# Optimization experiments

Hardware: AMD Instinct MI355X
Metric: run time of the kernel (lower is better)

## Reference

```python
import jax, jax.numpy as jnp
import numpy as np

HEAD_SIZE = 64


def setup_inputs() -> dict:
    key = jax.random.key(0)
    ks = jax.random.split(key, 4)
    B, S, H, D = 8, 4096, 768, HEAD_SIZE
    scale = 1.0 / np.sqrt(H)
    return {
        "x": jax.random.normal(ks[0], (B, S, H), dtype=jnp.float32),
        "Wq": jax.random.normal(ks[1], (H, D), dtype=jnp.float32) * scale,
        "bq": jnp.zeros((D,), dtype=jnp.float32),
        "Wk": jax.random.normal(ks[2], (H, D), dtype=jnp.float32) * scale,
        "bk": jnp.zeros((D,), dtype=jnp.float32),
        "Wv": jax.random.normal(ks[3], (H, D), dtype=jnp.float32) * scale,
        "bv": jnp.zeros((D,), dtype=jnp.float32),
    }


def reference(x, Wq, bq, Wk, bk, Wv, bv):
    # x: [B, S, H]
    B, S, H = x.shape
    D = Wq.shape[1]
    q = x @ Wq + bq  # [B, S, D]
    k = x @ Wk + bk
    v = x @ Wv + bv
    # naive full score matrix [B, S, S]
    scores = jnp.einsum("bsd,btd->bst", q, k)
    causal = jnp.tril(jnp.ones((S, S), dtype=bool))  # lower-triangular mask
    scores = jnp.where(causal[None, :, :], scores, -jnp.inf)
    attn = jax.nn.softmax(scores / jnp.sqrt(jnp.float32(D)), axis=-1)
    # dropout is identity in eval/deterministic reference
    out = jnp.einsum("bst,btd->bsd", attn, v)  # [B, S, D]
    return out
```

## Files before the change

### kernel.cpp

```cpp
#include <hip/hip_runtime.h>

typedef unsigned short u16;
typedef __bf16 bf16_t;
typedef bf16_t bf16x8 __attribute__((ext_vector_type(8)));
typedef float f32x4 __attribute__((ext_vector_type(4)));
typedef u16 u16x8 __attribute__((ext_vector_type(8)));
typedef u16 u16x4 __attribute__((ext_vector_type(4)));

#define B_ 8
#define S_ 4096
#define H_ 768
#define M_ (B_ * S_)

__device__ __forceinline__ u16 f2b(float f) {
  unsigned u = __float_as_uint(f);
  u += 0x7fffu + ((u >> 16) & 1u);
  return (u16)(u >> 16);
}

__device__ __forceinline__ void gl_lds16(const void* g, void* l) {
  __builtin_amdgcn_global_load_lds(
      (const __attribute__((address_space(1))) void*)g,
      (__attribute__((address_space(3))) void*)l, 16, 0, 0);
}

__global__ __launch_bounds__(256) void wconv_k(const float* __restrict__ Wq,
                                               const float* __restrict__ Wk,
                                               const float* __restrict__ Wv,
                                               u16* __restrict__ WbT) {
  __shared__ float wt[64 * 68];
  const int tid = threadIdx.x;
  int mat = blockIdx.x / 12;
  int k0 = (blockIdx.x % 12) * 64;
  const float* W = (mat == 0) ? Wq : ((mat == 1) ? Wk : Wv);
  int r = tid >> 2, c0 = (tid & 3) * 16;
  const float* src = W + (size_t)(k0 + r) * 64 + c0;
#pragma unroll
  for (int j = 0; j < 16; j += 4)
    *(float4*)&wt[r * 68 + c0 + j] = *(const float4*)(src + j);
  __syncthreads();
  int d = tid >> 2;
  u16* dst = WbT + (size_t)(mat * 64 + d) * 768 + k0 + c0;
  u16x8 o0, o1;
#pragma unroll
  for (int j = 0; j < 8; ++j) o0[j] = f2b(wt[(c0 + j) * 68 + d]);
#pragma unroll
  for (int j = 0; j < 8; ++j) o1[j] = f2b(wt[(c0 + 8 + j) * 68 + d]);
  *(u16x8*)dst = o0;
  *(u16x8*)(dst + 8) = o1;
}

__global__ __launch_bounds__(256) void qkv_k(const float* __restrict__ x,
                                             const u16* __restrict__ WbT,
                                             const float* __restrict__ bq,
                                             const float* __restrict__ bk,
                                             const float* __restrict__ bv,
                                             u16* __restrict__ qb,
                                             u16* __restrict__ kb,
                                             u16* __restrict__ vbT) {
  __shared__ __align__(16) u16 smem[2 * 2560 + 2 * 7680];
  const int tid = threadIdx.x;
  const int w = tid >> 6, ln = tid & 15, qd = (tid >> 4) & 3;
  const int row0 = blockIdx.x * 64;

  const f32x4 z4 = {0.f, 0.f, 0.f, 0.f};
  f32x4 acc[4][3];
#pragma unroll
  for (int rt = 0; rt < 4; ++rt)
#pragma unroll
    for (int ct = 0; ct < 3; ++ct) acc[rt][ct] = z4;

  const int xr = tid >> 2, xc = (tid & 3) * 8;
  float4 xf0, xf1;
  u16x8 wf[3];

  auto load_t = [&](int kt) {
    const float* sx = x + (size_t)(row0 + xr) * 768 + kt * 32 + xc;
    xf0 = *(const float4*)sx;
    xf1 = *(const float4*)(sx + 4);
#pragma unroll
    for (int i = 0; i < 3; ++i) {
      int c = i * 256 + tid;
      int r = c >> 2, off = (c & 3) * 8;
      wf[i] = *(const u16x8*)(WbT + (size_t)r * 768 + kt * 32 + off);
    }
  };

  load_t(0);
  for (int kt = 0; kt < 24; ++kt) {
    u16* xs = smem + (kt & 1) * 2560;
    u16* wsb = smem + 5120 + (kt & 1) * 7680;
    {
      u16x8 v;
      v[0] = f2b(xf0.x); v[1] = f2b(xf0.y); v[2] = f2b(xf0.z); v[3] = f2b(xf0.w);
      v[4] = f2b(xf1.x); v[5] = f2b(xf1.y); v[6] = f2b(xf1.z); v[7] = f2b(xf1.w);
      *(u16x8*)&xs[xr * 40 + xc] = v;
#pragma unroll
      for (int i = 0; i < 3; ++i) {
        int c = i * 256 + tid;
        int r = c >> 2, off = (c & 3) * 8;
        *(u16x8*)&wsb[r * 40 + off] = wf[i];
      }
    }
    if (kt < 23) load_t(kt + 1);
    __syncthreads();
    bf16x8 af[4], bfr[3];
#pragma unroll
    for (int rt = 0; rt < 4; ++rt)
      af[rt] = *(const bf16x8*)&xs[(rt * 16 + ln) * 40 + qd * 8];
#pragma unroll
    for (int ct = 0; ct < 3; ++ct)
      bfr[ct] = *(const bf16x8*)&wsb[(w * 48 + ct * 16 + ln) * 40 + qd * 8];
#pragma unroll
    for (int rt = 0; rt < 4; ++rt)
#pragma unroll
      for (int ct = 0; ct < 3; ++ct)
        acc[rt][ct] = __builtin_amdgcn_mfma_f32_16x16x32_bf16(
            af[rt], bfr[ct], acc[rt][ct], 0, 0, 0);
    __syncthreads();
  }

  u16* vt = smem;
#pragma unroll
  for (int ct = 0; ct < 3; ++ct) {
    int col = w * 48 + ct * 16 + ln;
    int mat = col >> 6, d = col & 63;
    if (mat < 2) {
      const float* bp = (mat == 0) ? bq : bk;
      u16* op = (mat == 0) ? qb : kb;
      float bias = bp[d];
      float scale = (mat == 0) ? 0.18033688011112042f : 1.0f;
#pragma unroll
      for (int rt = 0; rt < 4; ++rt)
#pragma unroll
        for (int r = 0; r < 4; ++r)
          op[(size_t)(row0 + rt * 16 + qd * 4 + r) * 64 + d] =
              f2b((acc[rt][ct][r] + bias) * scale);
    } else {
      float bias = bv[d];
#pragma unroll
      for (int rt = 0; rt < 4; ++rt)
#pragma unroll
        for (int r = 0; r < 4; ++r)
          vt[d * 72 + rt * 16 + qd * 4 + r] = f2b(acc[rt][ct][r] + bias);
    }
  }
  __syncthreads();
  {
    int d = tid >> 2, so = (tid & 3) * 16;
    int b = row0 >> 12, s0 = row0 & 4095;
    u16* dst = vbT + ((size_t)b * 64 + d) * 4096 + s0 + so;
    *(u16x8*)dst = *(const u16x8*)&vt[d * 72 + so];
    *(u16x8*)(dst + 8) = *(const u16x8*)&vt[d * 72 + so + 8];
  }
}

__global__ __launch_bounds__(256) void attn_k(const u16* __restrict__ qb,
                                              const u16* __restrict__ kb,
                                              const u16* __restrict__ vbT,
                                              float* __restrict__ po,
                                              float* __restrict__ pl) {
  __shared__ __align__(16) u16 ks[3][4096];
  __shared__ __align__(16) u16 vs[3][4096];
  __shared__ __align__(16) u16 ps[4 * 32 * 64];
  const int tid = threadIdx.x;
  const int wv = tid >> 6, ln = tid & 15, qd = (tid >> 4) & 3;
  const int id = blockIdx.x;
  const int b = id & 7;
  const int j = id >> 3;
  int qi = 31, acc = 0;
  while (acc + ((qi >> 3) + 1) <= j) {
    acc += (qi >> 3) + 1;
    --qi;
  }
  const int c = j - acc;
  const int ntiles = 2 * qi + 2;
  const int nc = (qi >> 3) + 1;
  const int bas = ntiles / nc, rem = ntiles % nc;
  const int tstart = c * bas + (c < rem ? c : rem);
  const int tcount = bas + (c < rem ? 1 : 0);
  const int q0 = qi * 128;
  const int q0w = q0 + wv * 32;
  const int base = b * S_;
  const u16* kg = kb + (size_t)base * 64;
  const u16* vg = vbT + (size_t)b * 64 * 4096;

  bf16x8 qf[2][2];
#pragma unroll
  for (int qt = 0; qt < 2; ++qt) {
    const u16* qrow = qb + (size_t)(base + q0w + qt * 16 + ln) * 64;
    qf[qt][0] = *(const bf16x8*)(qrow + qd * 8);
    qf[qt][1] = *(const bf16x8*)(qrow + 32 + qd * 8);
  }
  const f32x4 z4 = {0.f, 0.f, 0.f, 0.f};
  f32x4 o0[4] = {z4, z4, z4, z4};
  f32x4 o1[4] = {z4, z4, z4, z4};
  float lq0 = 0.f, lq1 = 0.f;
  u16* psw = ps + wv * 2048;
  const int sw = (ln & 7) << 3;
  const int lr = (tid & 63) >> 3, csl = tid & 7;

  auto prefetch = [&](int bufi, int tile) {
    const u16* kt_ = kg + (size_t)tile * 4096;
    const u16* vt_ = vg + tile * 64;
#pragma unroll
    for (int i = 0; i < 2; ++i) {
      int r0 = wv * 16 + i * 8;
      int r = r0 + lr;
      int cc = csl ^ (r & 7);
      gl_lds16(kt_ + r * 64 + cc * 8, &ks[bufi][r0 * 64]);
      gl_lds16(vt_ + (size_t)r * 4096 + cc * 8, &vs[bufi][r0 * 64]);
    }
  };

  prefetch(0, tstart);
  prefetch(1, tstart + (tcount > 1 ? 1 : 0));
  int cur = 0, pfb = 2;
  for (int it = 0; it < tcount; ++it) {
    asm volatile("s_waitcnt vmcnt(4)" ::: "memory");
    __builtin_amdgcn_s_barrier();
    int nx = it + 2;
    nx = nx < tcount ? nx : tcount - 1;
    prefetch(pfb, tstart + nx);
    const int t0a = (tstart + it) * 64;

    if (t0a <= q0w + 31) {
      f32x4 s0[4] = {z4, z4, z4, z4};
      f32x4 s1[4] = {z4, z4, z4, z4};
#pragma unroll
      for (int kc = 0; kc < 2; ++kc) {
        int cs = (kc * 4 + qd) ^ (ln & 7);
#pragma unroll
        for (int nt = 0; nt < 4; ++nt) {
          bf16x8 kf = *(const bf16x8*)&ks[cur][(nt * 16 + ln) * 64 + cs * 8];
          s0[nt] = __builtin_amdgcn_mfma_f32_16x16x32_bf16(kf, qf[0][kc], s0[nt], 0, 0, 0);
          s1[nt] = __builtin_amdgcn_mfma_f32_16x16x32_bf16(kf, qf[1][kc], s1[nt], 0, 0, 0);
        }
      }
      if (t0a + 63 > q0w) {
#pragma unroll
        for (int nt = 0; nt < 4; ++nt) {
          int tg = t0a + nt * 16 + qd * 4;
#pragma unroll
          for (int r = 0; r < 4; ++r) {
            if (tg + r > q0w + ln) s0[nt][r] = -INFINITY;
            if (tg + r > q0w + 16 + ln) s1[nt][r] = -INFINITY;
          }
        }
      }
#pragma unroll
      for (int nt = 0; nt < 4; ++nt) {
        u16x4 w0, w1;
#pragma unroll
        for (int r = 0; r < 4; ++r) {
          float p0 = __builtin_amdgcn_exp2f(s0[nt][r]);
          float p1 = __builtin_amdgcn_exp2f(s1[nt][r]);
          lq0 += p0;
          lq1 += p1;
          w0[r] = f2b(p0);
          w1[r] = f2b(p1);
        }
        int off = (nt * 16 + qd * 4) ^ sw;
        *(u16x4*)&psw[ln * 64 + off] = w0;
        *(u16x4*)&psw[(16 + ln) * 64 + off] = w1;
      }
#pragma unroll
      for (int kc = 0; kc < 2; ++kc) {
        int poff = (kc * 32 + qd * 8) ^ sw;
        bf16x8 a0 = *(const bf16x8*)&psw[ln * 64 + poff];
        bf16x8 a1 = *(const bf16x8*)&psw[(16 + ln) * 64 + poff];
        int cs = (kc * 4 + qd) ^ (ln & 7);
#pragma unroll
        for (int nt = 0; nt < 4; ++nt) {
          bf16x8 vf = *(const bf16x8*)&vs[cur][(nt * 16 + ln) * 64 + cs * 8];
          o0[nt] = __builtin_amdgcn_mfma_f32_16x16x32_bf16(a0, vf, o0[nt], 0, 0, 0);
          o1[nt] = __builtin_amdgcn_mfma_f32_16x16x32_bf16(a1, vf, o1[nt], 0, 0, 0);
        }
      }
    }
    cur = (cur == 2) ? 0 : cur + 1;
    pfb = (pfb == 2) ? 0 : pfb + 1;
  }

  lq0 += __shfl_xor(lq0, 16);
  lq0 += __shfl_xor(lq0, 32);
  lq1 += __shfl_xor(lq1, 16);
  lq1 += __shfl_xor(lq1, 32);

  float* op = po + (size_t)c * 2097152;
  float* lpt = pl + (size_t)c * 32768;
#pragma unroll
  for (int r = 0; r < 4; ++r) {
    int row0 = base + q0w + qd * 4 + r;
    int row1 = row0 + 16;
#pragma unroll
    for (int nt = 0; nt < 4; ++nt) {
      op[(size_t)row0 * 64 + nt * 16 + ln] = o0[nt][r];
      op[(size_t)row1 * 64 + nt * 16 + ln] = o1[nt][r];
    }
  }
  if (qd == 0) {
    lpt[base + q0w + ln] = lq0;
    lpt[base + q0w + 16 + ln] = lq1;
  }
}

__global__ __launch_bounds__(256) void comb_k(const float* __restrict__ po,
                                              const float* __restrict__ pl,
                                              float* __restrict__ out) {
  int idx = blockIdx.x * 256 + threadIdx.x;
  int r = idx >> 4, d0 = (idx & 15) * 4;
  int qi = (r & 4095) >> 7;
  int nc = (qi >> 3) + 1;
  const float* p = po + (size_t)r * 64 + d0;
  float4 a = *(const float4*)p;
  float l = pl[r];
  if (nc > 1) {
    float4 t = *(const float4*)(p + 2097152);
    a.x += t.x; a.y += t.y; a.z += t.z; a.w += t.w;
    l += pl[r + 32768];
  }
  if (nc > 2) {
    float4 t = *(const float4*)(p + 4194304);
    a.x += t.x; a.y += t.y; a.z += t.z; a.w += t.w;
    l += pl[r + 65536];
  }
  if (nc > 3) {
    float4 t = *(const float4*)(p + 6291456);
    a.x += t.x; a.y += t.y; a.z += t.z; a.w += t.w;
    l += pl[r + 98304];
  }
  float inv = 1.0f / l;
  a.x *= inv; a.y *= inv; a.z *= inv; a.w *= inv;
  *(float4*)(out + (size_t)r * 64 + d0) = a;
}

extern "C" void kernel_launch(void* const* d_in, const int* in_sizes, int n_in,
                              void* d_out, int out_size, void* d_ws, size_t ws_size,
                              hipStream_t stream) {
  const float* x  = (const float*)d_in[0];
  const float* Wq = (const float*)d_in[1];
  const float* bq = (const float*)d_in[2];
  const float* Wk = (const float*)d_in[3];
  const float* bk = (const float*)d_in[4];
  const float* Wv = (const float*)d_in[5];
  const float* bv = (const float*)d_in[6];
  float* out = (float*)d_out;

  char* wsp = (char*)d_ws;
  u16* WbT = (u16*)wsp;
  u16* qb  = (u16*)(wsp + 294912);
  u16* kb  = (u16*)(wsp + 4489216);
  u16* vbT = (u16*)(wsp + 8683520);
  float* po = (float*)(wsp + 12877824);
  float* pl = (float*)(wsp + 46432256);

  hipLaunchKernelGGL(wconv_k, dim3(36), dim3(256), 0, stream, Wq, Wk, Wv, WbT);
  hipLaunchKernelGGL(qkv_k, dim3(512), dim3(256), 0, stream,
                     x, WbT, bq, bk, bv, qb, kb, vbT);
  hipLaunchKernelGGL(attn_k, dim3(640), dim3(256), 0, stream,
                     qb, kb, vbT, po, pl);
  hipLaunchKernelGGL(comb_k, dim3(2048), dim3(256), 0, stream,
                     po, pl, out);
}
```

Before: 224.6 us.

## Keep softmax probabilities in registers by permuting V^T layout to match MFMA fragments

Removes the per-wave LDS round trip for the bf16 probability tile. The P values are now packed straight from the score accumulators into MFMA A operands with v_cvt_pk_bf16_f32. To make this valid, the projection kernel writes V^T with a permuted sequence order inside each 32-column group, so the register layout of P matches the K dimension of the PV MFMA. It also raises wave priority around the MFMA blocks with s_setprio. This relies on the column permutation being exactly consistent between the two kernels, and it frees the ps LDS buffer.

```diff
diff --git a/kernel.cpp b/kernel.cpp
--- a/kernel.cpp
+++ b/kernel.cpp
@@ -6,6 +6,7 @@
 typedef float f32x4 __attribute__((ext_vector_type(4)));
 typedef u16 u16x8 __attribute__((ext_vector_type(8)));
 typedef u16 u16x4 __attribute__((ext_vector_type(4)));
+typedef unsigned u32x4 __attribute__((ext_vector_type(4)));
 
 #define B_ 8
 #define S_ 4096
@@ -149,9 +150,13 @@
   {
     int d = tid >> 2, so = (tid & 3) * 16;
     int b = row0 >> 12, s0 = row0 & 4095;
-    u16* dst = vbT + ((size_t)b * 64 + d) * 4096 + s0 + so;
-    *(u16x8*)dst = *(const u16x8*)&vt[d * 72 + so];
-    *(u16x8*)(dst + 8) = *(const u16x8*)&vt[d * 72 + so + 8];
+    u16* dst = vbT + ((size_t)b * 64 + d) * 4096 + s0;
+#pragma unroll
+    for (int g = 0; g < 4; ++g) {
+      int ts = so + g * 4;
+      int tn = (ts & 0x23) | ((ts & 4) << 2) | ((ts & 0x18) >> 1);
+      *(u16x4*)(dst + ts) = *(const u16x4*)&vt[d * 72 + tn];
+    }
   }
 }
 
@@ -162,7 +167,6 @@
                                               float* __restrict__ pl) {
   __shared__ __align__(16) u16 ks[3][4096];
   __shared__ __align__(16) u16 vs[3][4096];
-  __shared__ __align__(16) u16 ps[4 * 32 * 64];
   const int tid = threadIdx.x;
   const int wv = tid >> 6, ln = tid & 15, qd = (tid >> 4) & 3;
   const int id = blockIdx.x;
@@ -196,8 +200,6 @@
   f32x4 o0[4] = {z4, z4, z4, z4};
   f32x4 o1[4] = {z4, z4, z4, z4};
   float lq0 = 0.f, lq1 = 0.f;
-  u16* psw = ps + wv * 2048;
-  const int sw = (ln & 7) << 3;
   const int lr = (tid & 63) >> 3, csl = tid & 7;
 
   auto prefetch = [&](int bufi, int tile) {
@@ -227,6 +229,7 @@
     if (t0a <= q0w + 31) {
       f32x4 s0[4] = {z4, z4, z4, z4};
       f32x4 s1[4] = {z4, z4, z4, z4};
+      __builtin_amdgcn_s_setprio(1);
 #pragma unroll
       for (int kc = 0; kc < 2; ++kc) {
         int cs = (kc * 4 + qd) ^ (ln & 7);
@@ -237,6 +240,7 @@
           s1[nt] = __builtin_amdgcn_mfma_f32_16x16x32_bf16(kf, qf[1][kc], s1[nt], 0, 0, 0);
         }
       }
+      __builtin_amdgcn_s_setprio(0);
       if (t0a + 63 > q0w) {
 #pragma unroll
         for (int nt = 0; nt < 4; ++nt) {
@@ -248,27 +252,32 @@
           }
         }
       }
-#pragma unroll
-      for (int nt = 0; nt < 4; ++nt) {
-        u16x4 w0, w1;
+      float p0[4][4], p1[4][4];
+#pragma unroll
+      for (int nt = 0; nt < 4; ++nt)
 #pragma unroll
         for (int r = 0; r < 4; ++r) {
-          float p0 = __builtin_amdgcn_exp2f(s0[nt][r]);
-          float p1 = __builtin_amdgcn_exp2f(s1[nt][r]);
-          lq0 += p0;
-          lq1 += p1;
-          w0[r] = f2b(p0);
-          w1[r] = f2b(p1);
+          p0[nt][r] = __builtin_amdgcn_exp2f(s0[nt][r]);
+          p1[nt][r] = __builtin_amdgcn_exp2f(s1[nt][r]);
+          lq0 += p0[nt][r];
+          lq1 += p1[nt][r];
         }
-        int off = (nt * 16 + qd * 4) ^ sw;
-        *(u16x4*)&psw[ln * 64 + off] = w0;
-        *(u16x4*)&psw[(16 + ln) * 64 + off] = w1;
-      }
+      unsigned pk0[8], pk1[8];
+#pragma unroll
+      for (int i = 0; i < 8; ++i) {
+        int nt = i >> 1, rb = (i & 1) * 2;
+        asm("v_cvt_pk_bf16_f32 %0, %1, %2"
+            : "=v"(pk0[i]) : "v"(p0[nt][rb]), "v"(p0[nt][rb + 1]));
+        asm("v_cvt_pk_bf16_f32 %0, %1, %2"
+            : "=v"(pk1[i]) : "v"(p1[nt][rb]), "v"(p1[nt][rb + 1]));
+      }
+      __builtin_amdgcn_s_setprio(1);
 #pragma unroll
       for (int kc = 0; kc < 2; ++kc) {
-        int poff = (kc * 32 + qd * 8) ^ sw;
-        bf16x8 a0 = *(const bf16x8*)&psw[ln * 64 + poff];
-        bf16x8 a1 = *(const bf16x8*)&psw[(16 + ln) * 64 + poff];
+        u32x4 w0 = {pk0[4 * kc], pk0[4 * kc + 1], pk0[4 * kc + 2], pk0[4 * kc + 3]};
+        u32x4 w1 = {pk1[4 * kc], pk1[4 * kc + 1], pk1[4 * kc + 2], pk1[4 * kc + 3]};
+        bf16x8 a0 = __builtin_bit_cast(bf16x8, w0);
+        bf16x8 a1 = __builtin_bit_cast(bf16x8, w1);
         int cs = (kc * 4 + qd) ^ (ln & 7);
 #pragma unroll
         for (int nt = 0; nt < 4; ++nt) {
@@ -277,6 +286,7 @@
           o1[nt] = __builtin_amdgcn_mfma_f32_16x16x32_bf16(a1, vf, o1[nt], 0, 0, 0);
         }
       }
+      __builtin_amdgcn_s_setprio(0);
     }
     cur = (cur == 2) ? 0 : cur + 1;
     pfb = (pfb == 2) ? 0 : pfb + 1;
```

After: 213.0 us. 5.1% less time.
